# Kernel tuning notes

Measured on AMD Instinct MI355X. Metric: run time of the kernel, lower is better.

The kernel has to match this reference:

```python
import jax, jax.numpy as jnp
import numpy as np

D_MODEL = 1024
N_HEADS = 16
D_K = D_MODEL // N_HEADS
D_FF = 4096
EPS = 1e-5


def _layernorm(x, g, b):
    mu = jnp.mean(x, axis=-1, keepdims=True)
    var = jnp.mean(jnp.square(x - mu), axis=-1, keepdims=True)
    return (x - mu) * jax.lax.rsqrt(var + EPS) * g + b


def setup_inputs() -> dict:
    key = jax.random.key(0)
    ks = jax.random.split(key, 16)
    s = 0.02
    B, S = 2, 2048
    inp = {
        "x": jax.random.normal(ks[0], (B, S, D_MODEL), dtype=jnp.float32),
        "mask": jnp.ones((1, 1, S, S), dtype=jnp.int32),
        # attention projections (stored [in, out]; y = x @ W + b)
        "Wq": jax.random.normal(ks[1], (D_MODEL, D_MODEL)) * s,
        "bq": jnp.zeros((D_MODEL,)),
        "Wk": jax.random.normal(ks[2], (D_MODEL, D_MODEL)) * s,
        "bk": jnp.zeros((D_MODEL,)),
        "Wv": jax.random.normal(ks[3], (D_MODEL, D_MODEL)) * s,
        "bv": jnp.zeros((D_MODEL,)),
        "Wo": jax.random.normal(ks[4], (D_MODEL, D_MODEL)) * s,
        "bo": jnp.zeros((D_MODEL,)),
        "temperature": jnp.sqrt(jnp.array([float(D_K)], dtype=jnp.float32)),
        "time_weights": jax.random.normal(ks[5], (1, N_HEADS, 1, D_K)),
        "gateW": jax.random.normal(ks[6], (D_K, 1)) * s,
        "gateb": jnp.zeros((1,)),
        "ln_attn_g": jnp.ones((D_MODEL,)),
        "ln_attn_b": jnp.zeros((D_MODEL,)),
        # feed-forward
        "fc1W": jax.random.normal(ks[7], (D_MODEL, D_FF)) * s,
        "fc1b": jnp.zeros((D_FF,)),
        "fc2W": jax.random.normal(ks[8], (D_FF, D_MODEL)) * s,
        "fc2b": jnp.zeros((D_MODEL,)),
        "n1g": jnp.ones((D_MODEL,)),
        "n1b": jnp.zeros((D_MODEL,)),
        "n2g": jnp.ones((D_MODEL,)),
        "n2b": jnp.zeros((D_MODEL,)),
    }
    return inp


def reference(x, mask, Wq, bq, Wk, bk, Wv, bv, Wo, bo, temperature,
              time_weights, gateW, gateb, ln_attn_g, ln_attn_b,
              fc1W, fc1b, fc2W, fc2b, n1g, n1b, n2g, n2b):
    B, S, D = x.shape
    H, dk = N_HEADS, D_K

    def heads(t):  # [B,S,D] -> [B,H,S,dk]
        return t.reshape(B, S, H, dk).transpose(0, 2, 1, 3)

    q = heads(x @ Wq + bq) + time_weights  # learned per-head bias on Q
    k = heads(x @ Wk + bk)
    v = heads(x @ Wv + bv)

    scores = jnp.einsum("bhqd,bhkd->bhqk", q, k) / temperature
    scores = jnp.where(mask == 0, jnp.float32(-1e9), scores)
    gate = jax.nn.sigmoid(q @ gateW + gateb)  # [B,H,S,1] per-query gate
    scores = scores * gate
    probs = jax.nn.softmax(scores, axis=-1)

    ctx = jnp.einsum("bhqk,bhkd->bhqd", probs, v)
    ctx = ctx.transpose(0, 2, 1, 3).reshape(B, S, D)
    attn_out = _layernorm(ctx @ Wo + bo, ln_attn_g, ln_attn_b)

    x1 = _layernorm(x + attn_out, n1g, n1b)
    ff = jax.nn.gelu(x1 @ fc1W + fc1b, approximate=False) @ fc2W + fc2b
    return _layernorm(x1 + ff, n2g, n2b)
```

## Files before the change

### kernel.cpp

```cpp
#include <hip/hip_runtime.h>
#include <stdint.h>
#include <math.h>


typedef uint16_t u16;
typedef unsigned long long u64;
typedef __attribute__((ext_vector_type(8))) short short8;
typedef __attribute__((ext_vector_type(4))) float f32x4;

#define S_LEN 2048
#define DM 1024

#define GLOAD_LDS16(g, l)                                                      \
  __builtin_amdgcn_global_load_lds(                                            \
      (const __attribute__((address_space(1))) void*)(g),                      \
      (__attribute__((address_space(3))) void*)(l), 16, 0, 0)

__device__ __forceinline__ float bf2f(u16 h) {
  union { uint32_t u; float f; } x;
  x.u = ((uint32_t)h) << 16;
  return x.f;
}
__device__ __forceinline__ u16 f2bf(float f) {
  union { float f; uint32_t u; } x;
  x.f = f;
  uint32_t r = (x.u + 0x7fffu + ((x.u >> 16) & 1u)) >> 16;
  return (u16)r;
}
__device__ __forceinline__ u16 f2bf_fast(float f) {
  union { float f; uint32_t u; } x;
  x.f = f;
  return (u16)((x.u + 0x8000u) >> 16);
}

union U8 { uint4 u; u16 s[8]; };
union U4 { uint2 u; u16 s[4]; };

__global__ __launch_bounds__(256) void cvt_k(const float* __restrict__ in,
                                             u16* __restrict__ out, int n) {
  int i = (blockIdx.x * 256 + threadIdx.x) * 4;
  if (i >= n) return;
  float4 v = *(const float4*)(in + i);
  U4 o;
  o.s[0] = f2bf(v.x); o.s[1] = f2bf(v.y); o.s[2] = f2bf(v.z); o.s[3] = f2bf(v.w);
  *(uint2*)(out + i) = o.u;
}

__global__ __launch_bounds__(256) void mb_k(const int* __restrict__ mask,
                                            u16* __restrict__ mb) {
  int tid = blockIdx.x * 256 + threadIdx.x;
  const int* src = mask + (size_t)tid * 16;
  uint32_t b = 0;
#pragma unroll
  for (int q = 0; q < 4; q++) {
    int4 m = *(const int4*)(src + q * 4);
    b |= (m.x != 0 ? 1u : 0u) << (q * 4 + 0);
    b |= (m.y != 0 ? 1u : 0u) << (q * 4 + 1);
    b |= (m.z != 0 ? 1u : 0u) << (q * 4 + 2);
    b |= (m.w != 0 ? 1u : 0u) << (q * 4 + 3);
  }
  mb[tid] = (u16)b;
}

__device__ __forceinline__ void tcvt_body(const float* __restrict__ in,
                                          u16* __restrict__ out, int R, int C) {
  __shared__ u16 tile[64][72];
  int c0 = blockIdx.x * 64, r0 = blockIdx.y * 64;
  int t = threadIdx.x;
  int r = t & 63, seg = t >> 6;
  const float* src = in + (size_t)(r0 + r) * C + c0 + seg * 16;
#pragma unroll
  for (int q = 0; q < 4; q++) {
    float4 v = *(const float4*)(src + q * 4);
    tile[r][seg * 16 + q * 4 + 0] = f2bf(v.x);
    tile[r][seg * 16 + q * 4 + 1] = f2bf(v.y);
    tile[r][seg * 16 + q * 4 + 2] = f2bf(v.z);
    tile[r][seg * 16 + q * 4 + 3] = f2bf(v.w);
  }
  __syncthreads();
  U8 v0, v1;
#pragma unroll
  for (int i = 0; i < 8; i++) v0.s[i] = tile[seg * 16 + i][r];
#pragma unroll
  for (int i = 0; i < 8; i++) v1.s[i] = tile[seg * 16 + 8 + i][r];
  u16* dst = out + (size_t)(c0 + r) * R + r0 + seg * 16;
  *(uint4*)dst = v0.u;
  *(uint4*)(dst + 8) = v1.u;
}

__global__ __launch_bounds__(256) void transpose_cvt_k(const float* __restrict__ in,
                                                       u16* __restrict__ out,
                                                       int R, int C) {
  tcvt_body(in, out, R, C);
}

__global__ __launch_bounds__(256) void transpose_cvt3_k(const float* __restrict__ i0,
                                                        const float* __restrict__ i1,
                                                        const float* __restrict__ i2,
                                                        u16* __restrict__ o0,
                                                        u16* __restrict__ o1,
                                                        u16* __restrict__ o2) {
  int z = blockIdx.z;
  const float* in = (z == 0) ? i0 : (z == 1) ? i1 : i2;
  u16* out = (z == 0) ? o0 : (z == 1) ? o1 : o2;
  tcvt_body(in, out, 1024, 1024);
}

__global__ __launch_bounds__(256) void vtrans_k(const u16* __restrict__ V,
                                                u16* __restrict__ VT) {
  __shared__ u16 tile[64][72];
  int bx = blockIdx.x, bh = blockIdx.y;
  int b = bh >> 4, h = bh & 15;
  int t = threadIdx.x, r = t & 63, seg = t >> 6;
  const u16* src = V + (size_t)(b * S_LEN + bx * 64 + r) * DM + h * 64 + seg * 16;
  *(uint4*)&tile[r][seg * 16] = *(const uint4*)src;
  *(uint4*)&tile[r][seg * 16 + 8] = *(const uint4*)(src + 8);
  __syncthreads();
  U8 v0, v1;
#pragma unroll
  for (int i = 0; i < 8; i++) v0.s[i] = tile[seg * 16 + i][r];
#pragma unroll
  for (int i = 0; i < 8; i++) v1.s[i] = tile[seg * 16 + 8 + i][r];
  u16* dst = VT + ((size_t)bh * 64 + r) * S_LEN + bx * 64 + seg * 16;
  *(uint4*)dst = v0.u;
  *(uint4*)(dst + 8) = v1.u;
}

template <int BM, int EPI, int MXS>
__global__ __launch_bounds__(256) void gemm_bt(const u16* __restrict__ A,
                                               const u16* __restrict__ Bt,
                                               u16* __restrict__ C,
                                               const float* __restrict__ bias,
                                               int M, int N, int K) {
  constexpr int MI = BM / 32;
  constexpr int RPW = BM / 4;
  __shared__ u16 As[BM * 32];
  __shared__ u16 Bs[128 * 32];
  int t = threadIdx.x;
  int wid = t >> 6, lane = t & 63;
  int g = lane >> 4, li = lane & 15;
  int bx = MXS ? blockIdx.y : blockIdx.x;
  int by = MXS ? blockIdx.x : blockIdx.y;
  int wr = (wid >> 1) * (BM / 2), wc = (wid & 1) * 64;

  const u16* a0 = A + (size_t)(by * BM + wid * RPW + (lane >> 2)) * K + (lane & 3) * 8;
  const u16* b0 = Bt + (size_t)(bx * 128 + wid * 32 + (lane >> 2)) * K + (lane & 3) * 8;
  u16* lA0 = &As[wid * RPW * 32];
  u16* lB0 = &Bs[wid * 1024];

  f32x4 acc[MI][4];
#pragma unroll
  for (int i = 0; i < MI; i++)
#pragma unroll
    for (int j = 0; j < 4; j++) acc[i][j] = (f32x4){0.f, 0.f, 0.f, 0.f};

  for (int k0 = 0; k0 < K; k0 += 32) {
    GLOAD_LDS16(a0 + k0, lA0);
    if (BM == 128) GLOAD_LDS16(a0 + (size_t)16 * K + k0, lA0 + 512);
    GLOAD_LDS16(b0 + k0, lB0);
    GLOAD_LDS16(b0 + (size_t)16 * K + k0, lB0 + 512);
    __syncthreads();
    short8 af[MI], bfv[4];
#pragma unroll
    for (int i = 0; i < MI; i++)
      af[i] = *(const short8*)&As[(wr + i * 16 + li) * 32 + g * 8];
#pragma unroll
    for (int i = 0; i < 4; i++)
      bfv[i] = *(const short8*)&Bs[(wc + i * 16 + li) * 32 + g * 8];
#pragma unroll
    for (int mi = 0; mi < MI; mi++)
#pragma unroll
      for (int ni = 0; ni < 4; ni++)
        acc[mi][ni] = __builtin_amdgcn_mfma_f32_16x16x32_bf16(
            af[mi], bfv[ni], acc[mi][ni], 0, 0, 0);
    __syncthreads();
  }

#pragma unroll
  for (int ni = 0; ni < 4; ni++) {
    int col = bx * 128 + wc + ni * 16 + li;
    float bv = bias[col];
#pragma unroll
    for (int mi = 0; mi < MI; mi++) {
#pragma unroll
      for (int r = 0; r < 4; r++) {
        int row = by * BM + wr + mi * 16 + g * 4 + r;
        float v = acc[mi][ni][r] + bv;
        if (EPI == 2) v = 0.5f * v * (1.0f + erff(v * 0.70710678118654752f));
        C[(size_t)row * N + col] = f2bf(v);
      }
    }
  }
}

__global__ __launch_bounds__(256) void qkv_gemm(const u16* __restrict__ A,
                                                const u16* __restrict__ WTq,
                                                const u16* __restrict__ WTk,
                                                const u16* __restrict__ WTv,
                                                u16* __restrict__ Cq,
                                                u16* __restrict__ Ck,
                                                u16* __restrict__ Cv,
                                                const float* __restrict__ bq,
                                                const float* __restrict__ bk,
                                                const float* __restrict__ bv,
                                                const float* __restrict__ tw) {
  const int K = 1024, N = 1024;
  __shared__ u16 As[128 * 32];
  __shared__ u16 Bs[128 * 32];
  int t = threadIdx.x;
  int wid = t >> 6, lane = t & 63;
  int g = lane >> 4, li = lane & 15;
  int by = blockIdx.x, bx = blockIdx.y, z = blockIdx.z;
  int wr = (wid >> 1) * 64, wc = (wid & 1) * 64;

  const u16* Bt = (z == 0) ? WTq : (z == 1) ? WTk : WTv;
  u16* C = (z == 0) ? Cq : (z == 1) ? Ck : Cv;
  const float* bias = (z == 0) ? bq : (z == 1) ? bk : bv;

  const u16* a0 = A + (size_t)(by * 128 + wid * 32 + (lane >> 2)) * K + (lane & 3) * 8;
  const u16* b0 = Bt + (size_t)(bx * 128 + wid * 32 + (lane >> 2)) * K + (lane & 3) * 8;
  u16* lA0 = &As[wid * 1024];
  u16* lB0 = &Bs[wid * 1024];

  f32x4 acc[4][4];
#pragma unroll
  for (int i = 0; i < 4; i++)
#pragma unroll
    for (int j = 0; j < 4; j++) acc[i][j] = (f32x4){0.f, 0.f, 0.f, 0.f};

  for (int k0 = 0; k0 < K; k0 += 32) {
    GLOAD_LDS16(a0 + k0, lA0);
    GLOAD_LDS16(a0 + (size_t)16 * K + k0, lA0 + 512);
    GLOAD_LDS16(b0 + k0, lB0);
    GLOAD_LDS16(b0 + (size_t)16 * K + k0, lB0 + 512);
    __syncthreads();
    short8 af[4], bfv[4];
#pragma unroll
    for (int i = 0; i < 4; i++)
      af[i] = *(const short8*)&As[(wr + i * 16 + li) * 32 + g * 8];
#pragma unroll
    for (int i = 0; i < 4; i++)
      bfv[i] = *(const short8*)&Bs[(wc + i * 16 + li) * 32 + g * 8];
#pragma unroll
    for (int mi = 0; mi < 4; mi++)
#pragma unroll
      for (int ni = 0; ni < 4; ni++)
        acc[mi][ni] = __builtin_amdgcn_mfma_f32_16x16x32_bf16(
            af[mi], bfv[ni], acc[mi][ni], 0, 0, 0);
    __syncthreads();
  }

#pragma unroll
  for (int ni = 0; ni < 4; ni++) {
    int col = bx * 128 + wc + ni * 16 + li;
    float bvv = bias[col];
    if (z == 0) bvv += tw[col];
#pragma unroll
    for (int mi = 0; mi < 4; mi++) {
#pragma unroll
      for (int r = 0; r < 4; r++) {
        int row = by * 128 + wr + mi * 16 + g * 4 + r;
        C[(size_t)row * N + col] = f2bf(acc[mi][ni][r] + bvv);
      }
    }
  }
}

__global__ __launch_bounds__(256) void attn_k(const u16* __restrict__ Q,
                                              const u16* __restrict__ Kp,
                                              const u16* __restrict__ VT,
                                              u16* __restrict__ CTX,
                                              const u16* __restrict__ mb,
                                              const float* __restrict__ gateW,
                                              const float* __restrict__ gateb,
                                              const float* __restrict__ temp) {
  __shared__ u16 Qs[64][72];
  __shared__ u16 Ks[64][72];
  __shared__ u16 Vs[64][72];
  __shared__ u16 Ps[4][16][72];
  __shared__ float gate_s[64];

  int blk = blockIdx.x;
  int bh = blk & 31, qt = blk >> 5;
  int b = bh >> 4, h = bh & 15;
  int t = threadIdx.x, wid = t >> 6, lane = t & 63;
  int g = lane >> 4, li = lane & 15;
  int sq0 = qt * 64;

  const u16* Qb  = Q + ((size_t)b * S_LEN) * DM + h * 64;
  const u16* Kb  = Kp + ((size_t)b * S_LEN) * DM + h * 64;
  const u16* VTb = VT + ((size_t)(b * 16 + h) * 64) * S_LEN;

  {
    int r = t >> 2, cs = (t & 3) * 16;
    const u16* src = Qb + (size_t)(sq0 + r) * DM + cs;
    *(uint4*)&Qs[r][cs] = *(const uint4*)src;
    *(uint4*)&Qs[r][cs + 8] = *(const uint4*)(src + 8);
  }
  __syncthreads();
  if (t < 64) {
    float acc = gateb[0];
#pragma unroll
    for (int d = 0; d < 64; d++) acc += bf2f(Qs[t][d]) * gateW[d];
    gate_s[t] = 1.f / (1.f + __expf(-acc));
  }
  __syncthreads();

  const float LOG2E = 1.4426950408889634f;
  float invt2 = LOG2E / temp[0];
  const float NEG2 = -1.0e9f * 1.4426950408889634f;
  short8 qf0 = *(const short8*)&Qs[wid * 16 + li][g * 8];
  short8 qf1 = *(const short8*)&Qs[wid * 16 + li][32 + g * 8];
  float gqs[4], ng[4];
  int sq[4];
#pragma unroll
  for (int r = 0; r < 4; r++) {
    float gq = gate_s[wid * 16 + g * 4 + r];
    gqs[r] = gq * invt2;
    ng[r] = NEG2 * gq;
    sq[r] = sq0 + wid * 16 + g * 4 + r;
  }

  float m_i[4], psl[4];
  f32x4 o[4];
#pragma unroll
  for (int r = 0; r < 4; r++) { m_i[r] = -1e30f; psl[r] = 0.f; }
#pragma unroll
  for (int n = 0; n < 4; n++) o[n] = (f32x4){0.f, 0.f, 0.f, 0.f};

  for (int kt = 0; kt < 32; kt++) {
    __syncthreads();
    {
      int r = t >> 2, cs = (t & 3) * 16;
      const u16* srcK = Kb + (size_t)(kt * 64 + r) * DM + cs;
      *(uint4*)&Ks[r][cs] = *(const uint4*)srcK;
      *(uint4*)&Ks[r][cs + 8] = *(const uint4*)(srcK + 8);
      const u16* srcV = VTb + (size_t)r * S_LEN + kt * 64 + cs;
      *(uint4*)&Vs[r][cs] = *(const uint4*)srcV;
      *(uint4*)&Vs[r][cs + 8] = *(const uint4*)(srcV + 8);
    }
    u64 bits[4];
#pragma unroll
    for (int r = 0; r < 4; r++)
      bits[r] = *(const u64*)(mb + (size_t)sq[r] * 128 + kt * 4);
    __syncthreads();

    f32x4 sc[4];
#pragma unroll
    for (int ni = 0; ni < 4; ni++) {
      sc[ni] = (f32x4){0.f, 0.f, 0.f, 0.f};
      short8 kf0 = *(const short8*)&Ks[ni * 16 + li][g * 8];
      short8 kf1 = *(const short8*)&Ks[ni * 16 + li][32 + g * 8];
      sc[ni] = __builtin_amdgcn_mfma_f32_16x16x32_bf16(qf0, kf0, sc[ni], 0, 0, 0);
      sc[ni] = __builtin_amdgcn_mfma_f32_16x16x32_bf16(qf1, kf1, sc[ni], 0, 0, 0);
    }

    float sval[4][4];
    float rmax[4] = {-1e30f, -1e30f, -1e30f, -1e30f};
    bool allm = ((bits[0] & bits[1] & bits[2] & bits[3]) == ~0ull);
    if (__all(allm)) {
#pragma unroll
      for (int ni = 0; ni < 4; ni++)
#pragma unroll
        for (int r = 0; r < 4; r++) {
          float s = sc[ni][r] * gqs[r];
          sval[ni][r] = s;
          rmax[r] = fmaxf(rmax[r], s);
        }
    } else {
      u64 bs[4];
#pragma unroll
      for (int r = 0; r < 4; r++) bs[r] = bits[r] >> li;
#pragma unroll
      for (int ni = 0; ni < 4; ni++)
#pragma unroll
        for (int r = 0; r < 4; r++) {
          float s = ((bs[r] >> (ni * 16)) & 1ull) ? sc[ni][r] * gqs[r] : ng[r];
          sval[ni][r] = s;
          rmax[r] = fmaxf(rmax[r], s);
        }
    }
#pragma unroll
    for (int off = 1; off < 16; off <<= 1)
#pragma unroll
      for (int r = 0; r < 4; r++)
        rmax[r] = fmaxf(rmax[r], __shfl_xor(rmax[r], off, 64));

    float alpha[4];
#pragma unroll
    for (int r = 0; r < 4; r++) {
      float mnew = fmaxf(m_i[r], rmax[r]);
      alpha[r] = __builtin_amdgcn_exp2f(m_i[r] - mnew);
      m_i[r] = mnew;
    }
    float pp[4] = {0.f, 0.f, 0.f, 0.f};
#pragma unroll
    for (int ni = 0; ni < 4; ni++)
#pragma unroll
      for (int r = 0; r < 4; r++) {
        float p = __builtin_amdgcn_exp2f(sval[ni][r] - m_i[r]);
        pp[r] += p;
        Ps[wid][g * 4 + r][ni * 16 + li] = f2bf_fast(p);
      }
#pragma unroll
    for (int r = 0; r < 4; r++) psl[r] = psl[r] * alpha[r] + pp[r];
#pragma unroll
    for (int n = 0; n < 4; n++)
#pragma unroll
      for (int r = 0; r < 4; r++) o[n][r] *= alpha[r];

    __builtin_amdgcn_wave_barrier();

    short8 pf0 = *(const short8*)&Ps[wid][li][g * 8];
    short8 pf1 = *(const short8*)&Ps[wid][li][32 + g * 8];
#pragma unroll
    for (int ni = 0; ni < 4; ni++) {
      short8 vf0 = *(const short8*)&Vs[ni * 16 + li][g * 8];
      short8 vf1 = *(const short8*)&Vs[ni * 16 + li][32 + g * 8];
      o[ni] = __builtin_amdgcn_mfma_f32_16x16x32_bf16(pf0, vf0, o[ni], 0, 0, 0);
      o[ni] = __builtin_amdgcn_mfma_f32_16x16x32_bf16(pf1, vf1, o[ni], 0, 0, 0);
    }
  }

  float linv[4];
#pragma unroll
  for (int r = 0; r < 4; r++) {
    float l = psl[r];
#pragma unroll
    for (int off = 1; off < 16; off <<= 1) l += __shfl_xor(l, off, 64);
    linv[r] = 1.f / l;
  }
#pragma unroll
  for (int ni = 0; ni < 4; ni++) {
    int col = h * 64 + ni * 16 + li;
#pragma unroll
    for (int r = 0; r < 4; r++) {
      size_t row = (size_t)b * S_LEN + sq[r];
      CTX[row * DM + col] = f2bf(o[ni][r] * linv[r]);
    }
  }
}

__device__ __forceinline__ void block_sum2(float& a, float& b, float* red, int t) {
#pragma unroll
  for (int off = 32; off > 0; off >>= 1) {
    a += __shfl_xor(a, off, 64);
    b += __shfl_xor(b, off, 64);
  }
  __syncthreads();
  if ((t & 63) == 0) {
    red[(t >> 6) * 2] = a;
    red[(t >> 6) * 2 + 1] = b;
  }
  __syncthreads();
  a = red[0] + red[2] + red[4] + red[6];
  b = red[1] + red[3] + red[5] + red[7];
}

__global__ __launch_bounds__(256) void ln1_k(const u16* __restrict__ po,
                                             const float* __restrict__ x,
                                             const float* __restrict__ g1,
                                             const float* __restrict__ b1,
                                             const float* __restrict__ g2,
                                             const float* __restrict__ b2,
                                             u16* __restrict__ x1) {
  __shared__ float red[8];
  int row = blockIdx.x, t = threadIdx.x;
  size_t base = (size_t)row * 1024 + t * 4;
  U4 pv; pv.u = *(const uint2*)(po + base);
  float v[4];
#pragma unroll
  for (int i = 0; i < 4; i++) v[i] = bf2f(pv.s[i]);
  float s1 = v[0] + v[1] + v[2] + v[3];
  float s2 = v[0]*v[0] + v[1]*v[1] + v[2]*v[2] + v[3]*v[3];
  block_sum2(s1, s2, red, t);
  float mu = s1 * (1.f / 1024.f);
  float rs = rsqrtf(s2 * (1.f / 1024.f) - mu * mu + 1e-5f);
  float4 xv = *(const float4*)(x + base);
  float4 g1v = *(const float4*)(g1 + t * 4);
  float4 b1v = *(const float4*)(b1 + t * 4);
  float w[4];
  w[0] = xv.x + ((v[0] - mu) * rs * g1v.x + b1v.x);
  w[1] = xv.y + ((v[1] - mu) * rs * g1v.y + b1v.y);
  w[2] = xv.z + ((v[2] - mu) * rs * g1v.z + b1v.z);
  w[3] = xv.w + ((v[3] - mu) * rs * g1v.w + b1v.w);
  s1 = w[0] + w[1] + w[2] + w[3];
  s2 = w[0]*w[0] + w[1]*w[1] + w[2]*w[2] + w[3]*w[3];
  block_sum2(s1, s2, red, t);
  mu = s1 * (1.f / 1024.f);
  rs = rsqrtf(s2 * (1.f / 1024.f) - mu * mu + 1e-5f);
  float4 g2v = *(const float4*)(g2 + t * 4);
  float4 b2v = *(const float4*)(b2 + t * 4);
  U4 ov;
  ov.s[0] = f2bf((w[0] - mu) * rs * g2v.x + b2v.x);
  ov.s[1] = f2bf((w[1] - mu) * rs * g2v.y + b2v.y);
  ov.s[2] = f2bf((w[2] - mu) * rs * g2v.z + b2v.z);
  ov.s[3] = f2bf((w[3] - mu) * rs * g2v.w + b2v.w);
  *(uint2*)(x1 + base) = ov.u;
}

__global__ __launch_bounds__(256) void ln2_k(const u16* __restrict__ y,
                                             const u16* __restrict__ x1,
                                             const float* __restrict__ g,
                                             const float* __restrict__ b,
                                             float* __restrict__ out) {
  __shared__ float red[8];
  int row = blockIdx.x, t = threadIdx.x;
  size_t base = (size_t)row * 1024 + t * 4;
  U4 yv; yv.u = *(const uint2*)(y + base);
  U4 xv; xv.u = *(const uint2*)(x1 + base);
  float w[4];
#pragma unroll
  for (int i = 0; i < 4; i++) w[i] = bf2f(yv.s[i]) + bf2f(xv.s[i]);
  float s1 = w[0] + w[1] + w[2] + w[3];
  float s2 = w[0]*w[0] + w[1]*w[1] + w[2]*w[2] + w[3]*w[3];
  block_sum2(s1, s2, red, t);
  float mu = s1 * (1.f / 1024.f);
  float rs = rsqrtf(s2 * (1.f / 1024.f) - mu * mu + 1e-5f);
  float4 gv = *(const float4*)(g + t * 4);
  float4 bv = *(const float4*)(b + t * 4);
  float4 ov;
  ov.x = (w[0] - mu) * rs * gv.x + bv.x;
  ov.y = (w[1] - mu) * rs * gv.y + bv.y;
  ov.z = (w[2] - mu) * rs * gv.z + bv.z;
  ov.w = (w[3] - mu) * rs * gv.w + bv.w;
  *(float4*)(out + base) = ov;
}

extern "C" void kernel_launch(void* const* d_in, const int* in_sizes, int n_in,
                              void* d_out, int out_size, void* d_ws, size_t ws_size,
                              hipStream_t stream) {
  (void)in_sizes; (void)n_in; (void)out_size;
  const float* x    = (const float*)d_in[0];
  const int*   mask = (const int*)d_in[1];
  const float* Wq = (const float*)d_in[2];  const float* bq = (const float*)d_in[3];
  const float* Wk = (const float*)d_in[4];  const float* bk = (const float*)d_in[5];
  const float* Wv = (const float*)d_in[6];  const float* bv = (const float*)d_in[7];
  const float* Wo = (const float*)d_in[8];  const float* bo = (const float*)d_in[9];
  const float* temp = (const float*)d_in[10];
  const float* tw   = (const float*)d_in[11];
  const float* gW   = (const float*)d_in[12]; const float* gb  = (const float*)d_in[13];
  const float* lag  = (const float*)d_in[14]; const float* lab = (const float*)d_in[15];
  const float* f1W  = (const float*)d_in[16]; const float* f1b = (const float*)d_in[17];
  const float* f2W  = (const float*)d_in[18]; const float* f2b = (const float*)d_in[19];
  const float* n1g  = (const float*)d_in[20]; const float* n1b = (const float*)d_in[21];
  const float* n2g  = (const float*)d_in[22]; const float* n2b = (const float*)d_in[23];
  float* out = (float*)d_out;

  u16* ws = (u16*)d_ws;
  const size_t MB4 = (size_t)4096 * 1024;
  u16* s0 = ws;
  u16* s1 = ws + 1 * MB4;
  u16* s2 = ws + 2 * MB4;
  u16* s3 = ws + 3 * MB4;
  u16* s4 = ws + 4 * MB4;
  u16* d0 = (u16*)d_out;
  u16* d1 = d0 + MB4;
  bool bigws = ws_size >= (size_t)9 * 8 * 1024 * 1024;
  u16* Hfull = ws + 5 * MB4;

  dim3 blk(256);
  cvt_k<<<dim3(4096), blk, 0, stream>>>(x, s4, 4096 * 1024);
  transpose_cvt3_k<<<dim3(16, 16, 3), blk, 0, stream>>>(Wq, Wk, Wv, s0, s1, s2);
  qkv_gemm<<<dim3(32, 8, 3), blk, 0, stream>>>(s4, s0, s1, s2, s3, d0, d1,
                                               bq, bk, bv, tw);
  vtrans_k<<<dim3(32, 32), blk, 0, stream>>>(d1, s0);
  mb_k<<<dim3(1024), blk, 0, stream>>>(mask, s1);
  transpose_cvt_k<<<dim3(16, 16), blk, 0, stream>>>(Wo, s4, 1024, 1024);
  attn_k<<<dim3(1024), blk, 0, stream>>>(s3, d0, s0, s2, s1, gW, gb, temp);
  gemm_bt<64, 0, 1><<<dim3(64, 8), blk, 0, stream>>>(s2, s4, d0, bo, 4096, 1024, 1024);
  ln1_k<<<dim3(4096), blk, 0, stream>>>(d0, x, lag, lab, n1g, n1b, s3);
  transpose_cvt_k<<<dim3(64, 16), blk, 0, stream>>>(f1W, s0, 1024, 4096);
  transpose_cvt_k<<<dim3(16, 64), blk, 0, stream>>>(f2W, s1, 4096, 1024);
  if (bigws) {
    gemm_bt<128, 2, 0><<<dim3(32, 32), blk, 0, stream>>>(s3, s0, Hfull, f1b,
                                                         4096, 4096, 1024);
    gemm_bt<64, 0, 0><<<dim3(8, 64), blk, 0, stream>>>(Hfull, s1, s2, f2b,
                                                       4096, 1024, 4096);
  } else {
    for (int i = 0; i < 2; i++) {
      const u16* Ai = s3 + (size_t)i * 2048 * 1024;
      u16* Yi = s2 + (size_t)i * 2048 * 1024;
      gemm_bt<128, 2, 0><<<dim3(32, 16), blk, 0, stream>>>(Ai, s0, d0, f1b,
                                                           2048, 4096, 1024);
      gemm_bt<64, 0, 1><<<dim3(32, 8), blk, 0, stream>>>(d0, s1, Yi, f2b,
                                                         2048, 1024, 4096);
    }
  }
  ln2_k<<<dim3(4096), blk, 0, stream>>>(s2, s3, n2g, n2b, out);
}
```

Measured before the change: 477.3 us.

## Double-buffer LDS in GEMM kernels and use fast polynomial GELU

```diff
diff --git a/kernel.cpp b/kernel.cpp
--- a/kernel.cpp
+++ b/kernel.cpp
@@ -15,6 +15,12 @@
   __builtin_amdgcn_global_load_lds(                                            \
       (const __attribute__((address_space(1))) void*)(g),                      \
       (__attribute__((address_space(3))) void*)(l), 16, 0, 0)
+
+#define VM0_BARRIER()                                                          \
+  do {                                                                         \
+    asm volatile("s_waitcnt vmcnt(0)" ::: "memory");                           \
+    __builtin_amdgcn_s_barrier();                                              \
+  } while (0)
 
 __device__ __forceinline__ float bf2f(u16 h) {
   union { uint32_t u; float f; } x;
@@ -31,6 +37,21 @@
   union { float f; uint32_t u; } x;
   x.f = f;
   return (u16)((x.u + 0x8000u) >> 16);
+}
+
+__device__ __forceinline__ float gelu_ex(float v) {
+  float x = fabsf(v) * 0.70710678118654752f;
+  float t = __builtin_amdgcn_rcpf(__builtin_fmaf(0.3275911f, x, 1.0f));
+  float p = 1.061405429f;
+  p = __builtin_fmaf(p, t, -1.453152027f);
+  p = __builtin_fmaf(p, t, 1.421413741f);
+  p = __builtin_fmaf(p, t, -0.284496736f);
+  p = __builtin_fmaf(p, t, 0.254829592f);
+  p = p * t;
+  float ex = __builtin_amdgcn_exp2f(-1.4426950408889634f * x * x);
+  float er = __builtin_fmaf(-p, ex, 1.0f);
+  er = (v < 0.f) ? -er : er;
+  return 0.5f * v * (1.0f + er);
 }
 
 union U8 { uint4 u; u16 s[8]; };
@@ -134,8 +155,8 @@
                                                int M, int N, int K) {
   constexpr int MI = BM / 32;
   constexpr int RPW = BM / 4;
-  __shared__ u16 As[BM * 32];
-  __shared__ u16 Bs[128 * 32];
+  __shared__ u16 As[2][BM * 32];
+  __shared__ u16 Bs[2][128 * 32];
   int t = threadIdx.x;
   int wid = t >> 6, lane = t & 63;
   int g = lane >> 4, li = lane & 15;
@@ -145,8 +166,8 @@
 
   const u16* a0 = A + (size_t)(by * BM + wid * RPW + (lane >> 2)) * K + (lane & 3) * 8;
   const u16* b0 = Bt + (size_t)(bx * 128 + wid * 32 + (lane >> 2)) * K + (lane & 3) * 8;
-  u16* lA0 = &As[wid * RPW * 32];
-  u16* lB0 = &Bs[wid * 1024];
+  u16* lA[2] = {&As[0][wid * RPW * 32], &As[1][wid * RPW * 32]};
+  u16* lB[2] = {&Bs[0][wid * 1024], &Bs[1][wid * 1024]};
 
   f32x4 acc[MI][4];
 #pragma unroll
@@ -154,26 +175,39 @@
 #pragma unroll
     for (int j = 0; j < 4; j++) acc[i][j] = (f32x4){0.f, 0.f, 0.f, 0.f};
 
-  for (int k0 = 0; k0 < K; k0 += 32) {
-    GLOAD_LDS16(a0 + k0, lA0);
-    if (BM == 128) GLOAD_LDS16(a0 + (size_t)16 * K + k0, lA0 + 512);
-    GLOAD_LDS16(b0 + k0, lB0);
-    GLOAD_LDS16(b0 + (size_t)16 * K + k0, lB0 + 512);
-    __syncthreads();
+  auto stage = [&](int buf, int kk) {
+    GLOAD_LDS16(a0 + kk, lA[buf]);
+    if (BM == 128) GLOAD_LDS16(a0 + (size_t)16 * K + kk, lA[buf] + 512);
+    GLOAD_LDS16(b0 + kk, lB[buf]);
+    GLOAD_LDS16(b0 + (size_t)16 * K + kk, lB[buf] + 512);
+  };
+  auto compute = [&](int buf) {
     short8 af[MI], bfv[4];
 #pragma unroll
     for (int i = 0; i < MI; i++)
-      af[i] = *(const short8*)&As[(wr + i * 16 + li) * 32 + g * 8];
+      af[i] = *(const short8*)&As[buf][(wr + i * 16 + li) * 32 + g * 8];
 #pragma unroll
     for (int i = 0; i < 4; i++)
-      bfv[i] = *(const short8*)&Bs[(wc + i * 16 + li) * 32 + g * 8];
+      bfv[i] = *(const short8*)&Bs[buf][(wc + i * 16 + li) * 32 + g * 8];
+    __builtin_amdgcn_s_setprio(1);
 #pragma unroll
     for (int mi = 0; mi < MI; mi++)
 #pragma unroll
       for (int ni = 0; ni < 4; ni++)
         acc[mi][ni] = __builtin_amdgcn_mfma_f32_16x16x32_bf16(
             af[mi], bfv[ni], acc[mi][ni], 0, 0, 0);
-    __syncthreads();
+    __builtin_amdgcn_s_setprio(0);
+  };
+
+  stage(0, 0);
+  VM0_BARRIER();
+  for (int k0 = 0; k0 < K; k0 += 64) {
+    stage(1, k0 + 32);
+    compute(0);
+    VM0_BARRIER();
+    if (k0 + 64 < K) stage(0, k0 + 64);
+    compute(1);
+    VM0_BARRIER();
   }
 
 #pragma unroll
@@ -186,7 +220,7 @@
       for (int r = 0; r < 4; r++) {
         int row = by * BM + wr + mi * 16 + g * 4 + r;
         float v = acc[mi][ni][r] + bv;
-        if (EPI == 2) v = 0.5f * v * (1.0f + erff(v * 0.70710678118654752f));
+        if (EPI == 2) v = gelu_ex(v);
         C[(size_t)row * N + col] = f2bf(v);
       }
     }
@@ -205,8 +239,8 @@
                                                 const float* __restrict__ bv,
                                                 const float* __restrict__ tw) {
   const int K = 1024, N = 1024;
-  __shared__ u16 As[128 * 32];
-  __shared__ u16 Bs[128 * 32];
+  __shared__ u16 As[2][128 * 32];
+  __shared__ u16 Bs[2][128 * 32];
   int t = threadIdx.x;
   int wid = t >> 6, lane = t & 63;
   int g = lane >> 4, li = lane & 15;
@@ -219,8 +253,8 @@
 
   const u16* a0 = A + (size_t)(by * 128 + wid * 32 + (lane >> 2)) * K + (lane & 3) * 8;
   const u16* b0 = Bt + (size_t)(bx * 128 + wid * 32 + (lane >> 2)) * K + (lane & 3) * 8;
-  u16* lA0 = &As[wid * 1024];
-  u16* lB0 = &Bs[wid * 1024];
+  u16* lA[2] = {&As[0][wid * 1024], &As[1][wid * 1024]};
+  u16* lB[2] = {&Bs[0][wid * 1024], &Bs[1][wid * 1024]};
 
   f32x4 acc[4][4];
 #pragma unroll
@@ -228,26 +262,39 @@
 #pragma unroll
     for (int j = 0; j < 4; j++) acc[i][j] = (f32x4){0.f, 0.f, 0.f, 0.f};
 
-  for (int k0 = 0; k0 < K; k0 += 32) {
-    GLOAD_LDS16(a0 + k0, lA0);
-    GLOAD_LDS16(a0 + (size_t)16 * K + k0, lA0 + 512);
-    GLOAD_LDS16(b0 + k0, lB0);
-    GLOAD_LDS16(b0 + (size_t)16 * K + k0, lB0 + 512);
-    __syncthreads();
+  auto stage = [&](int buf, int kk) {
+    GLOAD_LDS16(a0 + kk, lA[buf]);
+    GLOAD_LDS16(a0 + (size_t)16 * K + kk, lA[buf] + 512);
+    GLOAD_LDS16(b0 + kk, lB[buf]);
+    GLOAD_LDS16(b0 + (size_t)16 * K + kk, lB[buf] + 512);
+  };
+  auto compute = [&](int buf) {
     short8 af[4], bfv[4];
 #pragma unroll
     for (int i = 0; i < 4; i++)
-      af[i] = *(const short8*)&As[(wr + i * 16 + li) * 32 + g * 8];
+      af[i] = *(const short8*)&As[buf][(wr + i * 16 + li) * 32 + g * 8];
 #pragma unroll
     for (int i = 0; i < 4; i++)
-      bfv[i] = *(const short8*)&Bs[(wc + i * 16 + li) * 32 + g * 8];
+      bfv[i] = *(const short8*)&Bs[buf][(wc + i * 16 + li) * 32 + g * 8];
+    __builtin_amdgcn_s_setprio(1);
 #pragma unroll
     for (int mi = 0; mi < 4; mi++)
 #pragma unroll
       for (int ni = 0; ni < 4; ni++)
         acc[mi][ni] = __builtin_amdgcn_mfma_f32_16x16x32_bf16(
             af[mi], bfv[ni], acc[mi][ni], 0, 0, 0);
-    __syncthreads();
+    __builtin_amdgcn_s_setprio(0);
+  };
+
+  stage(0, 0);
+  VM0_BARRIER();
+  for (int k0 = 0; k0 < K; k0 += 64) {
+    stage(1, k0 + 32);
+    compute(0);
+    VM0_BARRIER();
+    if (k0 + 64 < K) stage(0, k0 + 64);
+    compute(1);
+    VM0_BARRIER();
   }
 
 #pragma unroll
```

Measured after the change: 461.3 us. 1.03x faster.
